# Kernel optimization log

Measured on AMD Instinct MI355X. Metric: run time of the kernel, lower is better.

The kernel has to match this reference:

```python
import jax, jax.numpy as jnp
import numpy as np
from jax import lax

IN_CH = 512
OUT_CH = 512
HEAD_DIM = 8
NUM_HEADS = IN_CH // HEAD_DIM  # 64
INNER = NUM_HEADS * HEAD_DIM   # 512
KSIZE = 5
EPS = 1e-15
BN_EPS = 1e-5
DN = ('NCHW', 'OIHW', 'NCHW')


def setup_inputs() -> dict:
    key = jax.random.key(0)
    ks = jax.random.split(key, 10)
    s = 0.02
    return {
        'hidden_states': jax.random.normal(ks[0], (4, IN_CH, 64, 64), jnp.float32),
        'wq': jax.random.normal(ks[1], (INNER, IN_CH), jnp.float32) * s,
        'wk': jax.random.normal(ks[2], (INNER, IN_CH), jnp.float32) * s,
        'wv': jax.random.normal(ks[3], (INNER, IN_CH), jnp.float32) * s,
        # depthwise conv: groups = 3*INNER, 1 in-channel per group
        'dw_kernel': jax.random.normal(ks[4], (3 * INNER, 1, KSIZE, KSIZE), jnp.float32) * s,
        # grouped 1x1 conv: groups = 3*NUM_HEADS -> 3*INNER/(3*NUM_HEADS)=HEAD_DIM in-ch/group
        'pw_kernel': jax.random.normal(ks[5], (3 * INNER, HEAD_DIM, 1, 1), jnp.float32) * s,
        # proj_out 1x1: in = INNER*(1+len(kernel_sizes)) = 2*INNER
        'proj_kernel': jax.random.normal(ks[6], (OUT_CH, 2 * INNER, 1, 1), jnp.float32) * s,
        'bn_gamma': jnp.ones((OUT_CH,), jnp.float32),
        'bn_beta': jnp.zeros((OUT_CH,), jnp.float32),
        'bn_mean': jnp.zeros((OUT_CH,), jnp.float32),
        'bn_var': jnp.ones((OUT_CH,), jnp.float32),
    }


def _forward(hidden_states, wq, wk, wv, dw_kernel, pw_kernel, proj_kernel,
             bn_gamma, bn_beta, bn_mean, bn_var):
    x = hidden_states  # [B,C,H,W]
    B, _, H, W = x.shape
    h = jnp.moveaxis(x, 1, -1)  # [B,H,W,C]
    q = h @ wq.T
    k = h @ wk.T
    v = h @ wv.T
    qkv = jnp.moveaxis(jnp.concatenate([q, k, v], axis=-1), -1, 1)  # [B,3*INNER,H,W]

    # multi-scale aggregation: depthwise 5x5 then grouped 1x1
    dw = lax.conv_general_dilated(qkv, dw_kernel, (1, 1), 'SAME',
                                  feature_group_count=3 * INNER, dimension_numbers=DN)
    pw = lax.conv_general_dilated(dw, pw_kernel, (1, 1), 'VALID',
                                  feature_group_count=3 * NUM_HEADS, dimension_numbers=DN)
    qkv_all = jnp.concatenate([qkv, pw], axis=1)  # [B, 2*3*INNER, H, W]

    # relu linear attention (fp32)
    N = H * W
    d = HEAD_DIM
    f = qkv_all.astype(jnp.float32).reshape(B, -1, 3 * d, N)  # [B, nh_total, 3d, N]
    query = jax.nn.relu(f[:, :, :d])
    key_ = jax.nn.relu(f[:, :, d:2 * d])
    value = f[:, :, 2 * d:]
    value_pad = jnp.concatenate([value, jnp.ones_like(value[:, :, :1])], axis=2)  # [B,nh,d+1,N]
    scores = jnp.einsum('bhdn,bhen->bhde', value_pad, key_)   # [B,nh,d+1,d]
    out = jnp.einsum('bhde,bhen->bhdn', scores, query)         # [B,nh,d+1,N]
    out = out[:, :, :-1] / (out[:, :, -1:] + EPS)
    out = out.reshape(B, -1, H, W).astype(qkv_all.dtype)        # [B, 2*INNER, H, W]

    # proj_out 1x1 conv + BatchNorm2d (eval mode, running stats)
    y = lax.conv_general_dilated(out, proj_kernel, (1, 1), 'VALID', dimension_numbers=DN)
    inv = bn_gamma / jnp.sqrt(bn_var + BN_EPS)
    y = y * inv[None, :, None, None] + (bn_beta - bn_mean * inv)[None, :, None, None]
    return y + x


def reference(hidden_states, wq, wk, wv, dw_kernel, pw_kernel, proj_kernel,
              bn_gamma, bn_beta, bn_mean, bn_var):
    return _forward(hidden_states, wq, wk, wv, dw_kernel, pw_kernel, proj_kernel,
                    bn_gamma, bn_beta, bn_mean, bn_var)
```

## Files before the change

### kernel.cpp

```cpp
#include <hip/hip_runtime.h>
#include <hip/hip_bf16.h>

typedef __hip_bfloat16 bf16;
typedef __attribute__((ext_vector_type(8))) short bf16x8;
typedef __attribute__((ext_vector_type(4))) float f32x4;

#define BATCH 4
#define CIN   512
#define HW    64
#define NPIX  4096
#define CALL  3072
#define NHEAD 128
#define EPS_LITE 1e-15f
#define BN_EPS   1e-5f
#define LDKB  40


__device__ __forceinline__ short f2bf(float f) {
    __hip_bfloat16 h = __float2bfloat16(f);
    short s; __builtin_memcpy(&s, &h, 2); return s;
}
__device__ __forceinline__ float bfl(unsigned u) {
    unsigned v = u << 16; float f; __builtin_memcpy(&f, &v, 4); return f;
}
__device__ __forceinline__ float bfh(unsigned u) {
    unsigned v = u & 0xffff0000u; float f; __builtin_memcpy(&f, &v, 4); return f;
}
__device__ __forceinline__ unsigned packbf(float a, float b) {
    return (unsigned)(unsigned short)f2bf(a) | ((unsigned)(unsigned short)f2bf(b) << 16);
}

__device__ __forceinline__ void gll16(const void* gsrc, void* ldst) {
    __builtin_amdgcn_global_load_lds(
        (const __attribute__((address_space(1))) unsigned int*)gsrc,
        (__attribute__((address_space(3))) unsigned int*)ldst, 16, 0, 0);
}

__global__ __launch_bounds__(256) void k_cvtw(const float* __restrict__ wq,
                                              const float* __restrict__ wk,
                                              const float* __restrict__ wv,
                                              const float* __restrict__ pj,
                                              bf16* __restrict__ Wbf,
                                              bf16* __restrict__ Pbf) {
    const int e = (blockIdx.x * 256 + threadIdx.x) * 4;
    const float* s; bf16* dst;
    if (e < 786432) {
        int o;
        if (e < 262144)      { s = wq; o = e; }
        else if (e < 524288) { s = wk; o = e - 262144; }
        else                 { s = wv; o = e - 524288; }
        f32x4 v = *(const f32x4*)(s + o);
        dst = Wbf + e;
        ushort2 a = make_ushort2((unsigned short)f2bf(v[0]), (unsigned short)f2bf(v[1]));
        ushort2 b = make_ushort2((unsigned short)f2bf(v[2]), (unsigned short)f2bf(v[3]));
        *(ushort2*)dst = a; *(ushort2*)(dst + 2) = b;
    } else {
        const int o = e - 786432;
        f32x4 v = *(const f32x4*)(pj + o);
        dst = Pbf + o;
        ushort2 a = make_ushort2((unsigned short)f2bf(v[0]), (unsigned short)f2bf(v[1]));
        ushort2 b = make_ushort2((unsigned short)f2bf(v[2]), (unsigned short)f2bf(v[3]));
        *(ushort2*)dst = a; *(ushort2*)(dst + 2) = b;
    }
}

template<bool XF32, int KD, bool PROJ>
__global__ __launch_bounds__(256) void k_gemm2(
        const void* __restrict__ Xv,
        const bf16* __restrict__ Wb,
        bf16* __restrict__ Obf,
        const float* __restrict__ gm, const float* __restrict__ bt,
        const float* __restrict__ mu, const float* __restrict__ va,
        const float* __restrict__ resid, float* __restrict__ Of)
{
    constexpr int NT = KD / 32;
    __shared__ short Ald[2][128 * 32];
    __shared__ short Bld[128 * LDKB];

    const int t    = threadIdx.x;
    const int lane = t & 63;
    const int w    = t >> 6;
    const int wm   = w >> 1;
    const int wn   = w & 1;
    const int n0   = blockIdx.x * 128;
    const int c0   = blockIdx.y * 128;
    const int b    = blockIdx.z;

    const int arow = lane >> 2;
    const int akg  = lane & 3;
    const bf16* abase = Wb + (size_t)(c0 + w * 32 + arow) * KD + akg * 8;

    auto gllA = [&](int s, int buf) {
#pragma unroll
        for (int q = 0; q < 2; ++q)
            gll16(abase + (size_t)q * 16 * KD + s * 32,
                  &Ald[buf][(w * 32 + q * 16) * 32]);
    };

    const int brow = t & 127;
    const int bkh  = t >> 7;
    const float* bxf = (const float*)Xv + ((size_t)b * KD + bkh * 16) * NPIX + n0 + brow;
    const unsigned short* bxh =
        (const unsigned short*)Xv + ((size_t)b * KD + bkh * 16) * NPIX + n0 + brow;

    float bregf[16]; unsigned short bregh[16];
    auto bload = [&](int s) {
        if (XF32) {
#pragma unroll
            for (int i = 0; i < 16; ++i) bregf[i] = bxf[((size_t)s * 32 + i) * NPIX];
        } else {
#pragma unroll
            for (int i = 0; i < 16; ++i) bregh[i] = bxh[((size_t)s * 32 + i) * NPIX];
        }
    };
    auto bwrite = [&]() {
        bf16x8 p0, p1;
        if (XF32) {
#pragma unroll
            for (int j = 0; j < 8; ++j) { p0[j] = f2bf(bregf[j]); p1[j] = f2bf(bregf[8 + j]); }
        } else {
#pragma unroll
            for (int j = 0; j < 8; ++j) { p0[j] = (short)bregh[j]; p1[j] = (short)bregh[8 + j]; }
        }
        *(bf16x8*)&Bld[brow * LDKB + bkh * 16]     = p0;
        *(bf16x8*)&Bld[brow * LDKB + bkh * 16 + 8] = p1;
    };

    f32x4 acc[4][4];
#pragma unroll
    for (int ms = 0; ms < 4; ++ms)
#pragma unroll
        for (int ns = 0; ns < 4; ++ns)
#pragma unroll
            for (int j = 0; j < 4; ++j) acc[ms][ns][j] = 0.f;

    gllA(0, 0);
    bload(0);

    const int l15 = lane & 15, l4 = lane >> 4;
    for (int s = 0; s < NT; ++s) {
        const int cur = s & 1;
        bwrite();
        __syncthreads();
        if (s + 1 < NT) {
            gllA(s + 1, cur ^ 1);
            bload(s + 1);
        }

        bf16x8 af[4], bv[4];
#pragma unroll
        for (int ms = 0; ms < 4; ++ms)
            af[ms] = *(const bf16x8*)&Ald[cur][(wm * 64 + ms * 16 + l15) * 32 + l4 * 8];
#pragma unroll
        for (int ns = 0; ns < 4; ++ns)
            bv[ns] = *(const bf16x8*)&Bld[(wn * 64 + ns * 16 + l15) * LDKB + l4 * 8];
#pragma unroll
        for (int ms = 0; ms < 4; ++ms)
#pragma unroll
            for (int ns = 0; ns < 4; ++ns)
                acc[ms][ns] = __builtin_amdgcn_mfma_f32_16x16x32_bf16(
                    af[ms], bv[ns], acc[ms][ns], 0, 0, 0);

        __syncthreads();
    }

    if (!PROJ) {
#pragma unroll
        for (int ms = 0; ms < 4; ++ms) {
            const int crow = c0 + wm * 64 + ms * 16 + l4 * 4;
#pragma unroll
            for (int ns = 0; ns < 4; ++ns) {
                const int ncol = n0 + wn * 64 + ns * 16 + l15;
#pragma unroll
                for (int j = 0; j < 4; ++j) {
                    bf16 h; short sv = f2bf(acc[ms][ns][j]);
                    __builtin_memcpy(&h, &sv, 2);
                    Obf[((size_t)b * CALL + crow + j) * NPIX + ncol] = h;
                }
            }
        }
    } else {
#pragma unroll
        for (int ms = 0; ms < 4; ++ms) {
            const int crow = c0 + wm * 64 + ms * 16 + l4 * 4;
#pragma unroll
            for (int j = 0; j < 4; ++j) {
                const int o = crow + j;
                const float inv = gm[o] / sqrtf(va[o] + BN_EPS);
                const float sh  = bt[o] - mu[o] * inv;
#pragma unroll
                for (int ns = 0; ns < 4; ++ns) {
                    const int ncol = n0 + wn * 64 + ns * 16 + l15;
                    const size_t idx = ((size_t)b * 512 + o) * NPIX + ncol;
                    Of[idx] = acc[ms][ns][j] * inv + sh + resid[idx];
                }
            }
        }
    }
}

__global__ __launch_bounds__(256) void k_dwpw(const float* __restrict__ dwk,
                                              const float* __restrict__ pwk,
                                              bf16* __restrict__ qkv_all) {
    __shared__ short in_lds[8 * 20 * 80];
    __shared__ short dw_lds[8 * 16 * 64];

    const int t  = threadIdx.x;
    const int g  = blockIdx.y;
    const int b  = blockIdx.z;
    const int y0 = blockIdx.x * 16;

    const bf16* src = qkv_all + ((size_t)b * CALL + g * 8) * NPIX;
#pragma unroll
    for (int i = 0; i < 7; ++i) {
        const int v = i * 256 + t;
        if (v < 1600) {
            const int ch  = v / 200;
            const int rem = v % 200;
            const int row = rem / 10;
            const int seg = rem % 10;
            const int grow = y0 + row - 2;
            uint4 val = make_uint4(0u, 0u, 0u, 0u);
            if (seg >= 1 && seg <= 8 && grow >= 0 && grow < HW)
                val = *(const uint4*)(src + (size_t)ch * NPIX + grow * HW + (seg - 1) * 8);
            *(uint4*)&in_lds[ch * 1600 + row * 80 + seg * 8] = val;
        }
    }

    const int lane = t & 63;
    const int w    = t >> 6;
    const int xb   = lane & 7;
    const int ch   = lane >> 3;
    const int x0   = xb * 8;

    float kc[25];
    {
        const float* kp = dwk + (size_t)(g * 8 + ch) * 25;
#pragma unroll
        for (int i = 0; i < 25; ++i) kc[i] = kp[i];
    }
    __syncthreads();

    float A[5][12];
    const short* cb = &in_lds[ch * 1600 + x0];

    auto loadrow = [&](int L, float* f) {
        const short* rp = cb + L * 80;
        uint2 lo = *(const uint2*)(rp + 4);
        uint4 md = *(const uint4*)(rp + 8);
        uint2 hi = *(const uint2*)(rp + 16);
        f[0]  = bfl(lo.y); f[1]  = bfh(lo.y);
        f[2]  = bfl(md.x); f[3]  = bfh(md.x);
        f[4]  = bfl(md.y); f[5]  = bfh(md.y);
        f[6]  = bfl(md.z); f[7]  = bfh(md.z);
        f[8]  = bfl(md.w); f[9]  = bfh(md.w);
        f[10] = bfl(hi.x); f[11] = bfh(hi.x);
    };

    const int r0 = w * 4;
    loadrow(r0 + 0, A[0]);
    loadrow(r0 + 1, A[1]);
    loadrow(r0 + 2, A[2]);
    loadrow(r0 + 3, A[3]);

#pragma unroll
    for (int ri = 0; ri < 4; ++ri) {
        loadrow(r0 + ri + 4, A[(ri + 4) % 5]);
        float acc[8];
#pragma unroll
        for (int i = 0; i < 8; ++i) acc[i] = 0.f;
#pragma unroll
        for (int dy = 0; dy < 5; ++dy) {
            const float* Ar = A[(ri + dy) % 5];
#pragma unroll
            for (int dx = 0; dx < 5; ++dx) {
                const float kv = kc[dy * 5 + dx];
#pragma unroll
                for (int i = 0; i < 8; ++i)
                    acc[i] += Ar[i + dx] * kv;
            }
        }
        uint4 pk;
        pk.x = packbf(acc[0], acc[1]);
        pk.y = packbf(acc[2], acc[3]);
        pk.z = packbf(acc[4], acc[5]);
        pk.w = packbf(acc[6], acc[7]);
        *(uint4*)&dw_lds[ch * 1024 + (r0 + ri) * 64 + x0] = pk;
    }
    __syncthreads();

    const float* pwb = pwk + (size_t)g * 64;
#pragma unroll
    for (int it = 0; it < 2; ++it) {
        const int p2 = (it * 256 + t) * 2;
        float v0[8], v1[8];
#pragma unroll
        for (int ci = 0; ci < 8; ++ci) {
            const unsigned u = *(const unsigned*)&dw_lds[ci * 1024 + p2];
            v0[ci] = bfl(u); v1[ci] = bfh(u);
        }
        bf16* op = qkv_all + ((size_t)b * CALL + 1536 + g * 8) * NPIX + y0 * HW + p2;
#pragma unroll
        for (int o = 0; o < 8; ++o) {
            float s0 = 0.f, s1 = 0.f;
#pragma unroll
            for (int ci = 0; ci < 8; ++ci) {
                const float wv = pwb[o * 8 + ci];
                s0 += wv * v0[ci]; s1 += wv * v1[ci];
            }
            *(unsigned*)(op + (size_t)o * NPIX) = packbf(s0, s1);
        }
    }
}

__global__ __launch_bounds__(64) void k_scores(const bf16* __restrict__ qkv_all,
                                               float* __restrict__ part) {
    const int lane = threadIdx.x;
    const int h = blockIdx.y;
    const int b = blockIdx.z;
    const bf16* base = qkv_all + ((size_t)b * CALL + h * 24) * NPIX;

    float acc[72];
#pragma unroll
    for (int i = 0; i < 72; ++i) acc[i] = 0.f;

    for (int it = 0; it < 4; ++it) {
        const int n = blockIdx.x * 512 + it * 128 + lane * 2;
        const bf16* p = base + n;
        float k0[8], k1[8], v0[8], v1[8];
#pragma unroll
        for (int e = 0; e < 8; ++e) {
            const unsigned u = *(const unsigned*)&p[(size_t)(8 + e) * NPIX];
            k0[e] = fmaxf(bfl(u), 0.f); k1[e] = fmaxf(bfh(u), 0.f);
        }
#pragma unroll
        for (int d = 0; d < 8; ++d) {
            const unsigned u = *(const unsigned*)&p[(size_t)(16 + d) * NPIX];
            v0[d] = bfl(u); v1[d] = bfh(u);
        }
#pragma unroll
        for (int d = 0; d < 9; ++d) {
            const float vd0 = (d < 8) ? v0[d] : 1.f;
            const float vd1 = (d < 8) ? v1[d] : 1.f;
#pragma unroll
            for (int e = 0; e < 8; ++e)
                acc[d * 8 + e] += vd0 * k0[e] + vd1 * k1[e];
        }
    }

    const int bh = b * NHEAD + h;
#pragma unroll
    for (int i = 0; i < 72; ++i) {
        float v = acc[i];
        for (int off = 32; off; off >>= 1) v += __shfl_xor(v, off, 64);
        if (lane == 0) part[((size_t)bh * 72 + i) * 8 + blockIdx.x] = v;
    }
}

__global__ __launch_bounds__(128) void k_scores2(const float* __restrict__ part,
                                                 float* __restrict__ scores) {
    const int bh = blockIdx.x;
    const int i = threadIdx.x;
    if (i < 72) {
        float s = 0.f;
#pragma unroll
        for (int ns = 0; ns < 8; ++ns) s += part[((size_t)bh * 72 + i) * 8 + ns];
        scores[(size_t)bh * 72 + i] = s;
    }
}

__global__ __launch_bounds__(256) void k_att(const bf16* __restrict__ qkv_all,
                                             const float* __restrict__ scores,
                                             bf16* __restrict__ att) {
    const int n2 = (blockIdx.x * 256 + threadIdx.x) * 2;
    const int h = blockIdx.y;
    const int b = blockIdx.z;

    const bf16* qb = qkv_all + ((size_t)b * CALL + h * 24) * NPIX + n2;
    float q0[8], q1[8];
#pragma unroll
    for (int e = 0; e < 8; ++e) {
        const unsigned u = *(const unsigned*)&qb[(size_t)e * NPIX];
        q0[e] = fmaxf(bfl(u), 0.f); q1[e] = fmaxf(bfh(u), 0.f);
    }

    const float* sp = scores + (size_t)(b * NHEAD + h) * 72;
    float n0[9], n1[9];
#pragma unroll
    for (int d = 0; d < 9; ++d) {
        float s0 = 0.f, s1 = 0.f;
#pragma unroll
        for (int e = 0; e < 8; ++e) {
            const float wv = sp[d * 8 + e];
            s0 += wv * q0[e]; s1 += wv * q1[e];
        }
        n0[d] = s0; n1[d] = s1;
    }
    const float i0 = 1.f / (n0[8] + EPS_LITE);
    const float i1 = 1.f / (n1[8] + EPS_LITE);
    bf16* op = att + ((size_t)b * 1024 + h * 8) * NPIX + n2;
#pragma unroll
    for (int d = 0; d < 8; ++d)
        *(unsigned*)(op + (size_t)d * NPIX) = packbf(n0[d] * i0, n1[d] * i1);
}

extern "C" void kernel_launch(void* const* d_in, const int* in_sizes, int n_in,
                              void* d_out, int out_size, void* d_ws, size_t ws_size,
                              hipStream_t stream) {
    const float* x   = (const float*)d_in[0];
    const float* wq  = (const float*)d_in[1];
    const float* wk  = (const float*)d_in[2];
    const float* wv  = (const float*)d_in[3];
    const float* dwk = (const float*)d_in[4];
    const float* pwk = (const float*)d_in[5];
    const float* pj  = (const float*)d_in[6];
    const float* gm  = (const float*)d_in[7];
    const float* bt  = (const float*)d_in[8];
    const float* mu  = (const float*)d_in[9];
    const float* va  = (const float*)d_in[10];
    float* out = (float*)d_out;

    char* ws = (char*)d_ws;
    bf16*  qkv_all = (bf16*)(ws);
    bf16*  att     = (bf16*)(ws + 100663296);
    float* part    = (float*)(ws + 134217728);
    float* scores  = (float*)(ws + 135397376);
    bf16*  Wbf     = (bf16*)(ws + 135544832);
    bf16*  Pbf     = (bf16*)(ws + 137117696);

    k_cvtw<<<dim3(1280), 256, 0, stream>>>(wq, wk, wv, pj, Wbf, Pbf);
    k_gemm2<true, 512, false><<<dim3(32, 12, BATCH), 256, 0, stream>>>(
        x, Wbf, qkv_all, nullptr, nullptr, nullptr, nullptr, nullptr, nullptr);
    k_dwpw   <<<dim3( 4, 192, BATCH), 256, 0, stream>>>(dwk, pwk, qkv_all);
    k_scores <<<dim3( 8, 128, BATCH),  64, 0, stream>>>(qkv_all, part);
    k_scores2<<<dim3(512), 128, 0, stream>>>(part, scores);
    k_att    <<<dim3( 8, 128, BATCH), 256, 0, stream>>>(qkv_all, scores, att);
    k_gemm2<false, 1024, true><<<dim3(32, 4, BATCH), 256, 0, stream>>>(
        att, Pbf, nullptr, gm, bt, mu, va, x, out);
}
```

Baseline: 191.9 us.

## Transpose GEMM B operands to pixel-major and load both via global_load_lds

Adds a kernel that converts x to bf16 in pixel-major [B,N,C] layout, and makes the attention kernel write its output pixel-major too. Both GEMMs can then stage A and B tiles with direct global-to-LDS 16-byte loads and double buffering, instead of strided per-element register loads and manual LDS writes. The projection GEMM now uses 64-row M tiles, which doubles its grid. The cost is an extra transpose pass over x and a workspace region shared by xT and attT, which is safe only because xT is dead before attT is written.

```diff
diff --git a/kernel.cpp b/kernel.cpp
--- a/kernel.cpp
+++ b/kernel.cpp
@@ -13,7 +13,6 @@
 #define NHEAD 128
 #define EPS_LITE 1e-15f
 #define BN_EPS   1e-5f
-#define LDKB  40
 
 
 __device__ __forceinline__ short f2bf(float f) {
@@ -29,7 +28,6 @@
 __device__ __forceinline__ unsigned packbf(float a, float b) {
     return (unsigned)(unsigned short)f2bf(a) | ((unsigned)(unsigned short)f2bf(b) << 16);
 }
-
 __device__ __forceinline__ void gll16(const void* gsrc, void* ldst) {
     __builtin_amdgcn_global_load_lds(
         (const __attribute__((address_space(1))) unsigned int*)gsrc,
@@ -51,22 +49,46 @@
         else                 { s = wv; o = e - 524288; }
         f32x4 v = *(const f32x4*)(s + o);
         dst = Wbf + e;
-        ushort2 a = make_ushort2((unsigned short)f2bf(v[0]), (unsigned short)f2bf(v[1]));
-        ushort2 b = make_ushort2((unsigned short)f2bf(v[2]), (unsigned short)f2bf(v[3]));
-        *(ushort2*)dst = a; *(ushort2*)(dst + 2) = b;
+        *(ushort2*)dst = make_ushort2((unsigned short)f2bf(v[0]), (unsigned short)f2bf(v[1]));
+        *(ushort2*)(dst + 2) = make_ushort2((unsigned short)f2bf(v[2]), (unsigned short)f2bf(v[3]));
     } else {
         const int o = e - 786432;
         f32x4 v = *(const f32x4*)(pj + o);
         dst = Pbf + o;
-        ushort2 a = make_ushort2((unsigned short)f2bf(v[0]), (unsigned short)f2bf(v[1]));
-        ushort2 b = make_ushort2((unsigned short)f2bf(v[2]), (unsigned short)f2bf(v[3]));
-        *(ushort2*)dst = a; *(ushort2*)(dst + 2) = b;
-    }
-}
-
-template<bool XF32, int KD, bool PROJ>
-__global__ __launch_bounds__(256) void k_gemm2(
-        const void* __restrict__ Xv,
+        *(ushort2*)dst = make_ushort2((unsigned short)f2bf(v[0]), (unsigned short)f2bf(v[1]));
+        *(ushort2*)(dst + 2) = make_ushort2((unsigned short)f2bf(v[2]), (unsigned short)f2bf(v[3]));
+    }
+}
+
+__global__ __launch_bounds__(256) void k_cvtx(const float* __restrict__ x,
+                                              bf16* __restrict__ xT) {
+    __shared__ short lds[64][72];
+    const int t   = threadIdx.x;
+    const int px0 = blockIdx.x * 64;
+    const int k0  = blockIdx.y * 64;
+    const int b   = blockIdx.z;
+
+    const int pr = t & 15, rr = t >> 4;
+#pragma unroll
+    for (int it = 0; it < 4; ++it) {
+        const int row = it * 16 + rr;
+        f32x4 v = *(const f32x4*)(x + (size_t)(b * CIN + k0 + row) * NPIX + px0 + pr * 4);
+#pragma unroll
+        for (int i = 0; i < 4; ++i) lds[pr * 4 + i][row] = f2bf(v[i]);
+    }
+    __syncthreads();
+
+    const int px = t >> 2, kc = t & 3;
+    uint4 u0 = *(const uint4*)&lds[px][kc * 16];
+    uint4 u1 = *(const uint4*)&lds[px][kc * 16 + 8];
+    bf16* dst = xT + ((size_t)b * NPIX + px0 + px) * 512 + k0 + kc * 16;
+    *(uint4*)dst = u0;
+    *(uint4*)(dst + 8) = u1;
+}
+
+template<int KD, int MT, bool PROJ>
+__global__ __launch_bounds__(256) void k_gemm3(
+        const bf16* __restrict__ Xt,
         const bf16* __restrict__ Wb,
         bf16* __restrict__ Obf,
         const float* __restrict__ gm, const float* __restrict__ bt,
@@ -74,88 +96,58 @@
         const float* __restrict__ resid, float* __restrict__ Of)
 {
     constexpr int NT = KD / 32;
-    __shared__ short Ald[2][128 * 32];
-    __shared__ short Bld[128 * LDKB];
+    constexpr int MS = MT / 32;
+    constexpr int AG = MT / 64;
+    __shared__ short Ald[2][MT * 32];
+    __shared__ short Bld[2][128 * 32];
 
     const int t    = threadIdx.x;
     const int lane = t & 63;
     const int w    = t >> 6;
-    const int wm   = w >> 1;
-    const int wn   = w & 1;
+    const int wm   = w >> 1, wn = w & 1;
     const int n0   = blockIdx.x * 128;
-    const int c0   = blockIdx.y * 128;
+    const int c0   = blockIdx.y * MT;
     const int b    = blockIdx.z;
 
-    const int arow = lane >> 2;
-    const int akg  = lane & 3;
-    const bf16* abase = Wb + (size_t)(c0 + w * 32 + arow) * KD + akg * 8;
-
-    auto gllA = [&](int s, int buf) {
+    const bf16* abase = Wb + (size_t)(c0 + w * (MT / 4) + (lane >> 2)) * KD + (lane & 3) * 8;
+    const bf16* bbase = Xt + ((size_t)b * NPIX + n0 + w * 32 + (lane >> 2)) * KD + (lane & 3) * 8;
+
+    auto stage = [&](int s, int buf) {
+#pragma unroll
+        for (int q = 0; q < AG; ++q)
+            gll16(abase + (size_t)q * 16 * KD + s * 32,
+                  &Ald[buf][(w * (MT / 4) + q * 16) * 32]);
 #pragma unroll
         for (int q = 0; q < 2; ++q)
-            gll16(abase + (size_t)q * 16 * KD + s * 32,
-                  &Ald[buf][(w * 32 + q * 16) * 32]);
+            gll16(bbase + (size_t)q * 16 * KD + s * 32,
+                  &Bld[buf][(w * 32 + q * 16) * 32]);
     };
 
-    const int brow = t & 127;
-    const int bkh  = t >> 7;
-    const float* bxf = (const float*)Xv + ((size_t)b * KD + bkh * 16) * NPIX + n0 + brow;
-    const unsigned short* bxh =
-        (const unsigned short*)Xv + ((size_t)b * KD + bkh * 16) * NPIX + n0 + brow;
-
-    float bregf[16]; unsigned short bregh[16];
-    auto bload = [&](int s) {
-        if (XF32) {
-#pragma unroll
-            for (int i = 0; i < 16; ++i) bregf[i] = bxf[((size_t)s * 32 + i) * NPIX];
-        } else {
-#pragma unroll
-            for (int i = 0; i < 16; ++i) bregh[i] = bxh[((size_t)s * 32 + i) * NPIX];
-        }
-    };
-    auto bwrite = [&]() {
-        bf16x8 p0, p1;
-        if (XF32) {
-#pragma unroll
-            for (int j = 0; j < 8; ++j) { p0[j] = f2bf(bregf[j]); p1[j] = f2bf(bregf[8 + j]); }
-        } else {
-#pragma unroll
-            for (int j = 0; j < 8; ++j) { p0[j] = (short)bregh[j]; p1[j] = (short)bregh[8 + j]; }
-        }
-        *(bf16x8*)&Bld[brow * LDKB + bkh * 16]     = p0;
-        *(bf16x8*)&Bld[brow * LDKB + bkh * 16 + 8] = p1;
-    };
-
-    f32x4 acc[4][4];
-#pragma unroll
-    for (int ms = 0; ms < 4; ++ms)
+    f32x4 acc[MS][4];
+#pragma unroll
+    for (int ms = 0; ms < MS; ++ms)
 #pragma unroll
         for (int ns = 0; ns < 4; ++ns)
 #pragma unroll
             for (int j = 0; j < 4; ++j) acc[ms][ns][j] = 0.f;
 
-    gllA(0, 0);
-    bload(0);
+    stage(0, 0);
+    __syncthreads();
 
     const int l15 = lane & 15, l4 = lane >> 4;
     for (int s = 0; s < NT; ++s) {
         const int cur = s & 1;
-        bwrite();
-        __syncthreads();
-        if (s + 1 < NT) {
-            gllA(s + 1, cur ^ 1);
-            bload(s + 1);
-        }
-
-        bf16x8 af[4], bv[4];
-#pragma unroll
-        for (int ms = 0; ms < 4; ++ms)
-            af[ms] = *(const bf16x8*)&Ald[cur][(wm * 64 + ms * 16 + l15) * 32 + l4 * 8];
+        if (s + 1 < NT) stage(s + 1, cur ^ 1);
+
+        bf16x8 af[MS], bv[4];
+#pragma unroll
+        for (int ms = 0; ms < MS; ++ms)
+            af[ms] = *(const bf16x8*)&Ald[cur][(wm * (MT / 2) + ms * 16 + l15) * 32 + l4 * 8];
 #pragma unroll
         for (int ns = 0; ns < 4; ++ns)
-            bv[ns] = *(const bf16x8*)&Bld[(wn * 64 + ns * 16 + l15) * LDKB + l4 * 8];
-#pragma unroll
-        for (int ms = 0; ms < 4; ++ms)
+            bv[ns] = *(const bf16x8*)&Bld[cur][(wn * 64 + ns * 16 + l15) * 32 + l4 * 8];
+#pragma unroll
+        for (int ms = 0; ms < MS; ++ms)
 #pragma unroll
             for (int ns = 0; ns < 4; ++ns)
                 acc[ms][ns] = __builtin_amdgcn_mfma_f32_16x16x32_bf16(
@@ -166,8 +158,8 @@
 
     if (!PROJ) {
 #pragma unroll
-        for (int ms = 0; ms < 4; ++ms) {
-            const int crow = c0 + wm * 64 + ms * 16 + l4 * 4;
+        for (int ms = 0; ms < MS; ++ms) {
+            const int crow = c0 + wm * (MT / 2) + ms * 16 + l4 * 4;
 #pragma unroll
             for (int ns = 0; ns < 4; ++ns) {
                 const int ncol = n0 + wn * 64 + ns * 16 + l15;
@@ -181,8 +173,8 @@
         }
     } else {
 #pragma unroll
-        for (int ms = 0; ms < 4; ++ms) {
-            const int crow = c0 + wm * 64 + ms * 16 + l4 * 4;
+        for (int ms = 0; ms < MS; ++ms) {
+            const int crow = c0 + wm * (MT / 2) + ms * 16 + l4 * 4;
 #pragma unroll
             for (int j = 0; j < 4; ++j) {
                 const int o = crow + j;
@@ -369,39 +361,35 @@
     }
 }
 
-__global__ __launch_bounds__(256) void k_att(const bf16* __restrict__ qkv_all,
-                                             const float* __restrict__ scores,
-                                             bf16* __restrict__ att) {
-    const int n2 = (blockIdx.x * 256 + threadIdx.x) * 2;
+__global__ __launch_bounds__(256) void k_att3(const bf16* __restrict__ qkv_all,
+                                              const float* __restrict__ scores,
+                                              bf16* __restrict__ attT) {
+    const int px = blockIdx.x * 256 + threadIdx.x;
     const int h = blockIdx.y;
     const int b = blockIdx.z;
 
-    const bf16* qb = qkv_all + ((size_t)b * CALL + h * 24) * NPIX + n2;
-    float q0[8], q1[8];
-#pragma unroll
-    for (int e = 0; e < 8; ++e) {
-        const unsigned u = *(const unsigned*)&qb[(size_t)e * NPIX];
-        q0[e] = fmaxf(bfl(u), 0.f); q1[e] = fmaxf(bfh(u), 0.f);
-    }
+    const bf16* qb = qkv_all + ((size_t)b * CALL + h * 24) * NPIX + px;
+    float q[8];
+#pragma unroll
+    for (int e = 0; e < 8; ++e)
+        q[e] = fmaxf(__bfloat162float(qb[(size_t)e * NPIX]), 0.f);
 
     const float* sp = scores + (size_t)(b * NHEAD + h) * 72;
-    float n0[9], n1[9];
+    float num[9];
 #pragma unroll
     for (int d = 0; d < 9; ++d) {
-        float s0 = 0.f, s1 = 0.f;
-#pragma unroll
-        for (int e = 0; e < 8; ++e) {
-            const float wv = sp[d * 8 + e];
-            s0 += wv * q0[e]; s1 += wv * q1[e];
-        }
-        n0[d] = s0; n1[d] = s1;
-    }
-    const float i0 = 1.f / (n0[8] + EPS_LITE);
-    const float i1 = 1.f / (n1[8] + EPS_LITE);
-    bf16* op = att + ((size_t)b * 1024 + h * 8) * NPIX + n2;
-#pragma unroll
-    for (int d = 0; d < 8; ++d)
-        *(unsigned*)(op + (size_t)d * NPIX) = packbf(n0[d] * i0, n1[d] * i1);
+        float s = 0.f;
+#pragma unroll
+        for (int e = 0; e < 8; ++e) s += sp[d * 8 + e] * q[e];
+        num[d] = s;
+    }
+    const float inv = 1.f / (num[8] + EPS_LITE);
+    uint4 pk;
+    pk.x = packbf(num[0] * inv, num[1] * inv);
+    pk.y = packbf(num[2] * inv, num[3] * inv);
+    pk.z = packbf(num[4] * inv, num[5] * inv);
+    pk.w = packbf(num[6] * inv, num[7] * inv);
+    *(uint4*)(attT + ((size_t)b * NPIX + px) * 1024 + h * 8) = pk;
 }
 
 extern "C" void kernel_launch(void* const* d_in, const int* in_sizes, int n_in,
@@ -422,19 +410,21 @@
 
     char* ws = (char*)d_ws;
     bf16*  qkv_all = (bf16*)(ws);
-    bf16*  att     = (bf16*)(ws + 100663296);
+    bf16*  attT    = (bf16*)(ws + 100663296);
+    bf16*  xT      = (bf16*)(ws + 100663296);
     float* part    = (float*)(ws + 134217728);
     float* scores  = (float*)(ws + 135397376);
     bf16*  Wbf     = (bf16*)(ws + 135544832);
     bf16*  Pbf     = (bf16*)(ws + 137117696);
 
     k_cvtw<<<dim3(1280), 256, 0, stream>>>(wq, wk, wv, pj, Wbf, Pbf);
-    k_gemm2<true, 512, false><<<dim3(32, 12, BATCH), 256, 0, stream>>>(
-        x, Wbf, qkv_all, nullptr, nullptr, nullptr, nullptr, nullptr, nullptr);
+    k_cvtx<<<dim3(64, 8, BATCH), 256, 0, stream>>>(x, xT);
+    k_gemm3<512, 128, false><<<dim3(32, 12, BATCH), 256, 0, stream>>>(
+        xT, Wbf, qkv_all, nullptr, nullptr, nullptr, nullptr, nullptr, nullptr);
     k_dwpw   <<<dim3( 4, 192, BATCH), 256, 0, stream>>>(dwk, pwk, qkv_all);
     k_scores <<<dim3( 8, 128, BATCH),  64, 0, stream>>>(qkv_all, part);
     k_scores2<<<dim3(512), 128, 0, stream>>>(part, scores);
-    k_att    <<<dim3( 8, 128, BATCH), 256, 0, stream>>>(qkv_all, scores, att);
-    k_gemm2<false, 1024, true><<<dim3(32, 4, BATCH), 256, 0, stream>>>(
-        att, Pbf, nullptr, gm, bt, mu, va, x, out);
-}
+    k_att3   <<<dim3(16, 128, BATCH), 256, 0, stream>>>(qkv_all, scores, attT);
+    k_gemm3<1024, 64, true><<<dim3(32, 8, BATCH), 256, 0, stream>>>(
+        attT, Pbf, nullptr, gm, bt, mu, va, x, out);
+}
```

After: 174.8 us. 8.9% less time.
